# Kernel tuning notes

Measured on AMD Instinct MI355X. Metric: run time of the kernel, lower is better.

The kernel has to match this reference:

```python
import jax, jax.numpy as jnp
import numpy as np

D_MODEL = 1024
N_HEAD = 16
HEAD_SIZE = D_MODEL // N_HEAD
BLOCK_SIZE = 1024
NORM_EPS = 1e-6
B, T = 4, 1024


def setup_inputs() -> dict:
    key = jax.random.key(0)
    ks = jax.random.split(key, 16)
    s = 0.02
    d, h = D_MODEL, 4 * D_MODEL
    return {
        "x":  jax.random.normal(ks[0], (B, T, d), jnp.float32),
        "Wq": jax.random.normal(ks[1], (d, d), jnp.float32) * s,
        "bq": jax.random.normal(ks[2], (d,), jnp.float32) * s,
        "Wk": jax.random.normal(ks[3], (d, d), jnp.float32) * s,
        "bk": jax.random.normal(ks[4], (d,), jnp.float32) * s,
        "Wv": jax.random.normal(ks[5], (d, d), jnp.float32) * s,
        "bv": jax.random.normal(ks[6], (d,), jnp.float32) * s,
        "Wp": jax.random.normal(ks[7], (d, d), jnp.float32) * s,
        "bp": jax.random.normal(ks[8], (d,), jnp.float32) * s,
        "gamma": jnp.ones((d,), jnp.float32),
        "W1": jax.random.normal(ks[9], (d, h), jnp.float32) * s,
        "b1": jax.random.normal(ks[10], (h,), jnp.float32) * s,
        "W2": jax.random.normal(ks[11], (h, d), jnp.float32) * s,
        "b2": jax.random.normal(ks[12], (d,), jnp.float32) * s,
    }


def _rmsnorm(x, gamma):
    ms = jnp.mean(jnp.square(x), axis=-1, keepdims=True)
    return x * jax.lax.rsqrt(ms + NORM_EPS) * gamma


def _attn(x, Wq, bq, Wk, bk, Wv, bv, Wp, bp, causal):
    b, t, c = x.shape
    q = (x @ Wq + bq).reshape(b, t, N_HEAD, HEAD_SIZE)
    k = (x @ Wk + bk).reshape(b, t, N_HEAD, HEAD_SIZE)
    v = (x @ Wv + bv).reshape(b, t, N_HEAD, HEAD_SIZE)
    # NOTE: source divides by head_size**(-0.5) -> multiply by sqrt(head_size)
    scores = jnp.einsum("bqhd,bkhd->bhqk", q, k) * (HEAD_SIZE ** 0.5)
    if causal:
        tril = jnp.tril(jnp.ones((t, t), bool))
        scores = jnp.where(tril, scores, -jnp.inf)
    att = jax.nn.softmax(scores, axis=-1)
    out = jnp.einsum("bhqk,bkhd->bqhd", att, v).reshape(b, t, c)
    return out @ Wp + bp


def _ffwd(x, W1, b1, W2, b2):
    return jax.nn.leaky_relu(x @ W1 + b1, negative_slope=0.1) @ W2 + b2


def reference(x, Wq, bq, Wk, bk, Wv, bv, Wp, bp, gamma, W1, b1, W2, b2):
    # x_out = x + self_att(norm(x), mask=False)
    a = x + _attn(_rmsnorm(x, gamma), Wq, bq, Wk, bk, Wv, bv, Wp, bp, False)
    # x_out = x + ffwd(norm(x_out))   <- residual from ORIGINAL x (faithful)
    b = x + _ffwd(_rmsnorm(a, gamma), W1, b1, W2, b2)
    # x = x_out + self_att(norm(x_out), mask=True)
    c = b + _attn(_rmsnorm(b, gamma), Wq, bq, Wk, bk, Wv, bv, Wp, bp, True)
    return c
```

## Files before the change

### kernel.cpp

```cpp
#include <hip/hip_runtime.h>
#include <cstdint>
#include <cstddef>

typedef __bf16 bf16_t;
typedef __attribute__((ext_vector_type(8))) __bf16 bf16x8;
typedef __attribute__((ext_vector_type(4))) __bf16 bf16x4;
typedef __attribute__((ext_vector_type(4))) float f32x4;

constexpr int D  = 1024;
constexpr int TT = 1024;
constexpr int BB = 4;
constexpr int NH = 16;
constexpr int HS = 64;
constexpr int MR = BB * TT;
constexpr int HF = 4096;

__device__ inline void gload_lds16(const bf16_t* g, bf16_t* l)
{
    __builtin_amdgcn_global_load_lds(
        (const __attribute__((address_space(1))) void*)g,
        (__attribute__((address_space(3))) void*)l, 16, 0, 0);
}

template<bool LO>
__global__ __launch_bounds__(256) void rmsnorm_kernel(const float* __restrict__ x,
                                                      const float* __restrict__ gamma,
                                                      bf16_t* __restrict__ oh,
                                                      bf16_t* __restrict__ ol)
{
    int row = blockIdx.x;
    int t   = threadIdx.x;
    const float* xr = x + (size_t)row * D;
    float4 xv = *(const float4*)(xr + t * 4);
    float ss = xv.x * xv.x + xv.y * xv.y + xv.z * xv.z + xv.w * xv.w;
#pragma unroll
    for (int m = 1; m < 64; m <<= 1) ss += __shfl_xor(ss, m, 64);
    __shared__ float part[4];
    if ((t & 63) == 0) part[t >> 6] = ss;
    __syncthreads();
    float tot   = part[0] + part[1] + part[2] + part[3];
    float scale = rsqrtf(tot * (1.0f / D) + 1e-6f);
    float4 gv = *(const float4*)(gamma + t * 4);
    float vals[4] = {xv.x * scale * gv.x, xv.y * scale * gv.y,
                     xv.z * scale * gv.z, xv.w * scale * gv.w};
    bf16x4 vh, vl;
#pragma unroll
    for (int j = 0; j < 4; ++j) {
        bf16_t h = (bf16_t)vals[j];
        vh[j] = h;
        vl[j] = (bf16_t)(vals[j] - (float)h);
    }
    *(bf16x4*)(oh + (size_t)row * D + t * 4) = vh;
    if (LO) *(bf16x4*)(ol + (size_t)row * D + t * 4) = vl;
}

__global__ __launch_bounds__(256) void concat_bias_kernel(const float* __restrict__ a,
                                                          const float* __restrict__ b,
                                                          const float* __restrict__ c,
                                                          float* __restrict__ o)
{
    int i = blockIdx.x * 256 + threadIdx.x;
    o[i] = i < 1024 ? a[i] : (i < 2048 ? b[i - 1024] : c[i - 2048]);
}

template<bool LO>
__global__ __launch_bounds__(256) void convw_kernel(const float* __restrict__ W,
                                                    bf16_t* __restrict__ dH,
                                                    bf16_t* __restrict__ dL,
                                                    int K, int N)
{
    __shared__ float sld[64][65];
    int t = threadIdx.x;
    int k0 = blockIdx.x * 64, n0 = blockIdx.y * 64;
    int kr = t >> 4, nc = (t & 15) * 4;
#pragma unroll
    for (int p = 0; p < 4; ++p) {
        int k = p * 16 + kr;
        float4 v = *(const float4*)(W + (size_t)(k0 + k) * N + n0 + nc);
        sld[k][nc] = v.x; sld[k][nc + 1] = v.y; sld[k][nc + 2] = v.z; sld[k][nc + 3] = v.w;
    }
    __syncthreads();
    int n = t >> 2, kh = (t & 3) * 16;
    bf16x8 h0, l0, h1, l1;
#pragma unroll
    for (int j = 0; j < 8; ++j) {
        float v = sld[kh + j][n];
        bf16_t h = (bf16_t)v;
        h0[j] = h; l0[j] = (bf16_t)(v - (float)h);
    }
#pragma unroll
    for (int j = 0; j < 8; ++j) {
        float v = sld[kh + 8 + j][n];
        bf16_t h = (bf16_t)v;
        h1[j] = h; l1[j] = (bf16_t)(v - (float)h);
    }
    size_t o = (size_t)(n0 + n) * K + k0 + kh;
    *(bf16x8*)(dH + o)     = h0;
    *(bf16x8*)(dH + o + 8) = h1;
    if (LO) {
        *(bf16x8*)(dL + o)     = l0;
        *(bf16x8*)(dL + o + 8) = l1;
    }
}

template<int TN, bool CM, bool ALO, bool WLO, int OUTM, bool RELU, bool RESID>
__global__ __launch_bounds__(256, 2) void gemm_kernel(
    const bf16_t* __restrict__ Ahp, const bf16_t* __restrict__ Alp,
    const bf16_t* __restrict__ Whp, const bf16_t* __restrict__ Wlp,
    const float* __restrict__ bias, const float* resid,
    float* outf, bf16_t* __restrict__ outh, bf16_t* __restrict__ outl,
    int N, int K)
{
    constexpr int NF = TN / 32;
    constexpr int AP = ALO ? 2 : 1;
    constexpr int WP = WLO ? 2 : 1;
    __shared__ bf16_t sA[AP][128][32];
    __shared__ bf16_t sW[WP][TN][32];

    int t = threadIdx.x;
    int l = t & 63, w = t >> 6;
    int lr = l & 15, lg = l >> 4;

    int gx  = gridDim.x;
    int gy  = gridDim.y;
    int nwg = gx * gy;
    int bid = blockIdx.y * gx + blockIdx.x;
    int xcd = bid & 7, idx = bid >> 3;
    int nb, mb;
    if (CM) {
        int cw = gx >> 3;
        mb = idx % gy;
        nb = xcd * cw + idx / gy;
    } else {
        int s = xcd * (nwg >> 3) + idx;
        nb = s % gx; mb = s / gx;
    }
    int m0 = mb * 128, n0 = nb * TN;
    int wr = (w >> 1) * 64, wc = (w & 1) * (TN / 2);

    f32x4 acc[4][NF] = {};

    int srow = (l >> 2);
    int sch  = l & 3;

    for (int kk = 0; kk < K; kk += 32) {
        __syncthreads();
#pragma unroll
        for (int c = 0; c < 2; ++c) {
            int rbase = w * 32 + c * 16;
            int row = rbase + srow;
            int f = (row >> 1) & 3;
            size_t goff = (size_t)row * K + kk + (size_t)((sch ^ f)) * 8;
            gload_lds16(Ahp + (size_t)m0 * K + goff, &sA[0][rbase][0]);
            if (ALO) gload_lds16(Alp + (size_t)m0 * K + goff, &sA[AP - 1][rbase][0]);
        }
#pragma unroll
        for (int c = 0; c < TN / 64; ++c) {
            int rbase = w * (TN / 4) + c * 16;
            int row = rbase + srow;
            int f = (row >> 1) & 3;
            size_t goff = (size_t)row * K + kk + (size_t)((sch ^ f)) * 8;
            gload_lds16(Whp + (size_t)n0 * K + goff, &sW[0][rbase][0]);
            if (WLO) gload_lds16(Wlp + (size_t)n0 * K + goff, &sW[WP - 1][rbase][0]);
        }
        __syncthreads();

        bf16x8 a0[4], a1[4], b0[NF], b1[NF];
#pragma unroll
        for (int m = 0; m < 4; ++m) {
            int row = wr + m * 16 + lr;
            int sl = lg ^ ((row >> 1) & 3);
            a0[m] = *(const bf16x8*)&sA[0][row][sl * 8];
            if (ALO) a1[m] = *(const bf16x8*)&sA[AP - 1][row][sl * 8];
        }
#pragma unroll
        for (int n = 0; n < NF; ++n) {
            int row = wc + n * 16 + lr;
            int sl = lg ^ ((row >> 1) & 3);
            b0[n] = *(const bf16x8*)&sW[0][row][sl * 8];
            if (WLO) b1[n] = *(const bf16x8*)&sW[WP - 1][row][sl * 8];
        }
#pragma unroll
        for (int m = 0; m < 4; ++m)
#pragma unroll
            for (int n = 0; n < NF; ++n)
                acc[m][n] = __builtin_amdgcn_mfma_f32_16x16x32_bf16(a0[m], b0[n], acc[m][n], 0, 0, 0);
        if (WLO) {
#pragma unroll
            for (int m = 0; m < 4; ++m)
#pragma unroll
                for (int n = 0; n < NF; ++n)
                    acc[m][n] = __builtin_amdgcn_mfma_f32_16x16x32_bf16(a0[m], b1[n], acc[m][n], 0, 0, 0);
        }
        if (ALO) {
#pragma unroll
            for (int m = 0; m < 4; ++m)
#pragma unroll
                for (int n = 0; n < NF; ++n)
                    acc[m][n] = __builtin_amdgcn_mfma_f32_16x16x32_bf16(a1[m], b0[n], acc[m][n], 0, 0, 0);
        }
    }

#pragma unroll
    for (int m = 0; m < 4; ++m) {
#pragma unroll
        for (int n = 0; n < NF; ++n) {
            int col = n0 + wc + n * 16 + lr;
            float bv = bias[col];
#pragma unroll
            for (int r = 0; r < 4; ++r) {
                int row = m0 + wr + m * 16 + lg * 4 + r;
                float v = acc[m][n][r] + bv;
                if (RELU)  v = (v >= 0.0f) ? v : 0.1f * v;
                if (RESID) v += resid[(size_t)row * N + col];
                if (OUTM == 0) {
                    outf[(size_t)row * N + col] = v;
                } else if (OUTM == 2) {
                    outh[(size_t)row * N + col] = (bf16_t)v;
                } else {
                    bf16_t h = (bf16_t)v;
                    outh[(size_t)row * N + col] = h;
                    if (OUTM == 1 || col < 2048)
                        outl[(size_t)row * N + col] = (bf16_t)(v - (float)h);
                }
            }
        }
    }
}

template<bool CAUSAL>
__global__ __launch_bounds__(256, 2) void attn_kernel(
    const bf16_t* __restrict__ qkvH, const bf16_t* __restrict__ qkvL,
    bf16_t* __restrict__ oh)
{
    __shared__ bf16_t Vth[2][64][70];
    __shared__ bf16_t Ph[4][32][70];

    int tid = threadIdx.x;
    int b = blockIdx.z;
    int qb, h;
    if (CAUSAL) {
        int y = blockIdx.y;
        qb = (blockIdx.z & 2) ? (7 - (y & 7)) : (y & 7);
        h  = (blockIdx.x << 1) | (y >> 3);
    } else {
        h  = blockIdx.x;
        qb = blockIdx.y;
    }
    int l = tid & 63, w = tid >> 6;
    int lr = l & 15, lg = l >> 4;
    int qbase = qb * 128;
    const int QS = 3 * D;

    bf16x8 aqh[2][2], aql[2][2];
#pragma unroll
    for (int m = 0; m < 2; ++m) {
        size_t qoff = (size_t)(b * TT + qbase + w * 32 + m * 16 + lr) * QS + h * HS;
#pragma unroll
        for (int c = 0; c < 2; ++c) {
            aqh[m][c] = *(const bf16x8*)(qkvH + qoff + c * 32 + lg * 8);
            aql[m][c] = *(const bf16x8*)(qkvL + qoff + c * 32 + lg * 8);
        }
    }

    float mrow[2][4], lsum[2][4];
    f32x4 acc_o[2][4] = {};
#pragma unroll
    for (int m = 0; m < 2; ++m)
#pragma unroll
        for (int r = 0; r < 4; ++r) { mrow[m][r] = -1e30f; lsum[m][r] = 0.0f; }

    int ktmax = CAUSAL ? (2 * qb + 1) : (TT / 64 - 1);

    int vrow = tid >> 3;
    int vcol = (tid & 7) * 8;

    bf16x8 vreg[2];
#pragma unroll
    for (int rr = 0; rr < 2; ++rr)
        vreg[rr] = *(const bf16x8*)(qkvH + (size_t)(b * TT + vrow + rr * 32) * QS + 2 * D + h * HS + vcol);
#pragma unroll
    for (int rr = 0; rr < 2; ++rr)
#pragma unroll
        for (int j = 0; j < 8; ++j) Vth[0][vcol + j][vrow + rr * 32] = vreg[rr][j];

    bf16x8 kh0[4], kl0[4], kh1[4], kl1[4];
    {
        size_t koff = (size_t)(b * TT + lr) * QS + D + h * HS;
#pragma unroll
        for (int nt = 0; nt < 4; ++nt) {
            size_t ko = koff + (size_t)(nt * 16) * QS;
            kh0[nt] = *(const bf16x8*)(qkvH + ko + lg * 8);
            kl0[nt] = *(const bf16x8*)(qkvL + ko + lg * 8);
            kh1[nt] = *(const bf16x8*)(qkvH + ko + 32 + lg * 8);
            kl1[nt] = *(const bf16x8*)(qkvL + ko + 32 + lg * 8);
        }
    }
    __syncthreads();
    int cur = 0;

    for (int kt = 0; kt <= ktmax; ++kt) {
        int kbase = kt * 64;
        int ktn = kt < ktmax ? kt + 1 : ktmax;

#pragma unroll
        for (int rr = 0; rr < 2; ++rr)
            vreg[rr] = *(const bf16x8*)(qkvH + (size_t)(b * TT + ktn * 64 + vrow + rr * 32) * QS + 2 * D + h * HS + vcol);

        f32x4 accs[2][4];
#pragma unroll
        for (int nt = 0; nt < 4; ++nt) {
            __builtin_amdgcn_s_setprio(1);
#pragma unroll
            for (int m = 0; m < 2; ++m) {
                f32x4 s = {};
                s = __builtin_amdgcn_mfma_f32_16x16x32_bf16(aqh[m][0], kh0[nt], s, 0, 0, 0);
                s = __builtin_amdgcn_mfma_f32_16x16x32_bf16(aqh[m][0], kl0[nt], s, 0, 0, 0);
                s = __builtin_amdgcn_mfma_f32_16x16x32_bf16(aql[m][0], kh0[nt], s, 0, 0, 0);
                s = __builtin_amdgcn_mfma_f32_16x16x32_bf16(aqh[m][1], kh1[nt], s, 0, 0, 0);
                s = __builtin_amdgcn_mfma_f32_16x16x32_bf16(aqh[m][1], kl1[nt], s, 0, 0, 0);
                s = __builtin_amdgcn_mfma_f32_16x16x32_bf16(aql[m][1], kh1[nt], s, 0, 0, 0);
                accs[m][nt] = s * 8.0f;
            }
            __builtin_amdgcn_s_setprio(0);
        }

        {
            size_t koffn = (size_t)(b * TT + ktn * 64 + lr) * QS + D + h * HS;
#pragma unroll
            for (int nt = 0; nt < 4; ++nt) {
                size_t ko = koffn + (size_t)(nt * 16) * QS;
                kh0[nt] = *(const bf16x8*)(qkvH + ko + lg * 8);
                kl0[nt] = *(const bf16x8*)(qkvL + ko + lg * 8);
                kh1[nt] = *(const bf16x8*)(qkvH + ko + 32 + lg * 8);
                kl1[nt] = *(const bf16x8*)(qkvL + ko + 32 + lg * 8);
            }
        }

        if (CAUSAL && kt >= 2 * qb) {
#pragma unroll
            for (int m = 0; m < 2; ++m)
#pragma unroll
                for (int nt = 0; nt < 4; ++nt)
#pragma unroll
                    for (int r = 0; r < 4; ++r) {
                        int qrow = qbase + w * 32 + m * 16 + lg * 4 + r;
                        int kcol = kbase + nt * 16 + lr;
                        if (kcol > qrow) accs[m][nt][r] = -1e30f;
                    }
        }

#pragma unroll
        for (int m = 0; m < 2; ++m) {
            float alpha[4];
#pragma unroll
            for (int r = 0; r < 4; ++r) {
                float mx = fmaxf(fmaxf(accs[m][0][r], accs[m][1][r]),
                                 fmaxf(accs[m][2][r], accs[m][3][r]));
#pragma unroll
                for (int msk = 1; msk < 16; msk <<= 1) mx = fmaxf(mx, __shfl_xor(mx, msk, 64));
                float mnew = fmaxf(mrow[m][r], mx);
                float sum = 0.0f;
#pragma unroll
                for (int nt = 0; nt < 4; ++nt) {
                    float p = __expf(accs[m][nt][r] - mnew);
                    accs[m][nt][r] = p;
                    sum += p;
                }
#pragma unroll
                for (int msk = 1; msk < 16; msk <<= 1) sum += __shfl_xor(sum, msk, 64);
                alpha[r] = __expf(mrow[m][r] - mnew);
                lsum[m][r] = lsum[m][r] * alpha[r] + sum;
                mrow[m][r] = mnew;
            }
#pragma unroll
            for (int et = 0; et < 4; ++et)
#pragma unroll
                for (int r = 0; r < 4; ++r) acc_o[m][et][r] *= alpha[r];

#pragma unroll
            for (int nt = 0; nt < 4; ++nt)
#pragma unroll
                for (int r = 0; r < 4; ++r)
                    Ph[w][m * 16 + lg * 4 + r][nt * 16 + lr] = (bf16_t)accs[m][nt][r];
        }

#pragma unroll
        for (int m = 0; m < 2; ++m) {
            bf16x8 ap0 = *(const bf16x8*)&Ph[w][m * 16 + lr][lg * 8];
            bf16x8 ap1 = *(const bf16x8*)&Ph[w][m * 16 + lr][32 + lg * 8];
            __builtin_amdgcn_s_setprio(1);
#pragma unroll
            for (int et = 0; et < 4; ++et) {
                bf16x8 bv0 = *(const bf16x8*)&Vth[cur][et * 16 + lr][lg * 8];
                bf16x8 bv1 = *(const bf16x8*)&Vth[cur][et * 16 + lr][32 + lg * 8];
                acc_o[m][et] = __builtin_amdgcn_mfma_f32_16x16x32_bf16(ap0, bv0, acc_o[m][et], 0, 0, 0);
                acc_o[m][et] = __builtin_amdgcn_mfma_f32_16x16x32_bf16(ap1, bv1, acc_o[m][et], 0, 0, 0);
            }
            __builtin_amdgcn_s_setprio(0);
        }

#pragma unroll
        for (int rr = 0; rr < 2; ++rr)
#pragma unroll
            for (int j = 0; j < 8; ++j) Vth[cur ^ 1][vcol + j][vrow + rr * 32] = vreg[rr][j];
        __syncthreads();
        cur ^= 1;
    }

#pragma unroll
    for (int m = 0; m < 2; ++m) {
        size_t obase = (size_t)(b * TT + qbase + w * 32 + m * 16) * D + h * HS;
#pragma unroll
        for (int r = 0; r < 4; ++r) {
            float inv = 1.0f / lsum[m][r];
#pragma unroll
            for (int et = 0; et < 4; ++et) {
                float v = acc_o[m][et][r] * inv;
                size_t idx = obase + (size_t)(lg * 4 + r) * D + et * 16 + lr;
                oh[idx] = (bf16_t)v;
            }
        }
    }
}

extern "C" void kernel_launch(void* const* d_in, const int* in_sizes, int n_in,
                              void* d_out, int out_size, void* d_ws, size_t ws_size,
                              hipStream_t stream)
{
    const float* x     = (const float*)d_in[0];
    const float* Wq    = (const float*)d_in[1];
    const float* bq    = (const float*)d_in[2];
    const float* Wk    = (const float*)d_in[3];
    const float* bk    = (const float*)d_in[4];
    const float* Wv    = (const float*)d_in[5];
    const float* bv    = (const float*)d_in[6];
    const float* Wp    = (const float*)d_in[7];
    const float* bp    = (const float*)d_in[8];
    const float* gamma = (const float*)d_in[9];
    const float* W1    = (const float*)d_in[10];
    const float* b1    = (const float*)d_in[11];
    const float* W2    = (const float*)d_in[12];
    const float* b2    = (const float*)d_in[13];
    float* out = (float*)d_out;

    char* base = (char*)d_ws;
    bf16_t* nrmH  = (bf16_t*)(base);
    bf16_t* nrmL  = (bf16_t*)(base + (8u  << 20));
    bf16_t* qkvH  = (bf16_t*)(base + (16u << 20));
    bf16_t* qkvL  = (bf16_t*)(base + (40u << 20));
    bf16_t* h1H   = (bf16_t*)(base + (16u << 20));
    bf16_t* w1sl  = (bf16_t*)(base + (48u << 20));
    float*  bias3 = (float*)(base + (64u << 20));
    bf16_t* w2sl  = (bf16_t*)(base + (64u << 20));
    bf16_t* wsl   = (bf16_t*)(base + (80u << 20));
    bf16_t* aoH = nrmH;
    float* abuf = out;
    float* bbuf = out;

    size_t DD = (size_t)D * D;
    bf16_t* wqkvH = wsl;
    bf16_t* wqkvL = wsl + 3 * DD;
    bf16_t* wpH   = wsl + 6 * DD;
    bf16_t* wpL   = wsl + 7 * DD;

    dim3 blk(256);
    dim3 gcvD(D / 64, D / 64);
    dim3 gcv1(D / 64, HF / 64);
    dim3 gcv2(HF / 64, D / 64);
    dim3 gQKV(3 * D / 128, MR / 128);
    dim3 gP(D / 64, MR / 128);
    dim3 gF(HF / 128, MR / 128);
    dim3 gAnc(NH, TT / 128, BB);
    dim3 gAc(TT / 128, NH, BB);

    rmsnorm_kernel<true><<<MR, blk, 0, stream>>>(x, gamma, nrmH, nrmL);
    concat_bias_kernel<<<12, blk, 0, stream>>>(bq, bk, bv, bias3);
    convw_kernel<true><<<gcvD, blk, 0, stream>>>(Wq, wqkvH,          wqkvL,          D, D);
    convw_kernel<true><<<gcvD, blk, 0, stream>>>(Wk, wqkvH + DD,     wqkvL + DD,     D, D);
    convw_kernel<true><<<gcvD, blk, 0, stream>>>(Wv, wqkvH + 2 * DD, wqkvL + 2 * DD, D, D);
    convw_kernel<true><<<gcvD, blk, 0, stream>>>(Wp, wpH,            wpL,            D, D);
    gemm_kernel<128, false, true, true, 3, false, false><<<gQKV, blk, 0, stream>>>(nrmH, nrmL, wqkvH, wqkvL, bias3, nullptr, nullptr, qkvH, qkvL, 3 * D, D);
    attn_kernel<false><<<gAnc, blk, 0, stream>>>(qkvH, qkvL, aoH);
    gemm_kernel<64, false, false, true, 0, false, true><<<gP, blk, 0, stream>>>(aoH, nullptr, wpH, wpL, bp, x, abuf, nullptr, nullptr, D, D);

    rmsnorm_kernel<false><<<MR, blk, 0, stream>>>(abuf, gamma, nrmH, nullptr);
    convw_kernel<false><<<gcv1, blk, 0, stream>>>(W1, w1sl, nullptr, D, HF);
    gemm_kernel<128, true, false, false, 2, true, false><<<gF, blk, 0, stream>>>(nrmH, nullptr, w1sl, nullptr, b1, nullptr, nullptr, h1H, nullptr, HF, D);
    convw_kernel<false><<<gcv2, blk, 0, stream>>>(W2, w2sl, nullptr, HF, D);
    gemm_kernel<64, false, false, false, 0, false, true><<<gP, blk, 0, stream>>>(h1H, nullptr, w2sl, nullptr, b2, x, bbuf, nullptr, nullptr, D, HF);

    rmsnorm_kernel<true><<<MR, blk, 0, stream>>>(bbuf, gamma, nrmH, nrmL);
    concat_bias_kernel<<<12, blk, 0, stream>>>(bq, bk, bv, bias3);
    gemm_kernel<128, false, true, true, 3, false, false><<<gQKV, blk, 0, stream>>>(nrmH, nrmL, wqkvH, wqkvL, bias3, nullptr, nullptr, qkvH, qkvL, 3 * D, D);
    attn_kernel<true><<<gAc, blk, 0, stream>>>(qkvH, qkvL, aoH);
    gemm_kernel<64, false, false, true, 0, false, true><<<gP, blk, 0, stream>>>(aoH, nullptr, wpH, wpL, bp, bbuf, out, nullptr, nullptr, D, D);
}
```

Measured before the change: 522.7 us.

## Split V projection out of QKV GEMM and drop low-bf16 terms for V and Wp

The fused QKV projection becomes a split-precision QK GEMM plus a separate single-bf16 V GEMM writing its own buffer, and the attention kernel reads V from that buffer. The Wv and Wp weights are now converted only to high bf16 parts, and the output projection GEMM drops the low-weight correction term. This removes the extra MFMA passes and low-part memory traffic for V and the projections, at the cost of lower accuracy on those paths and one extra kernel launch per attention block.

```diff
diff --git a/kernel.cpp b/kernel.cpp
--- a/kernel.cpp
+++ b/kernel.cpp
@@ -56,11 +56,10 @@
 
 __global__ __launch_bounds__(256) void concat_bias_kernel(const float* __restrict__ a,
                                                           const float* __restrict__ b,
-                                                          const float* __restrict__ c,
                                                           float* __restrict__ o)
 {
     int i = blockIdx.x * 256 + threadIdx.x;
-    o[i] = i < 1024 ? a[i] : (i < 2048 ? b[i - 1024] : c[i - 2048]);
+    o[i] = i < 1024 ? a[i] : b[i - 1024];
 }
 
 template<bool LO>
@@ -220,8 +219,7 @@
                 } else {
                     bf16_t h = (bf16_t)v;
                     outh[(size_t)row * N + col] = h;
-                    if (OUTM == 1 || col < 2048)
-                        outl[(size_t)row * N + col] = (bf16_t)(v - (float)h);
+                    outl[(size_t)row * N + col] = (bf16_t)(v - (float)h);
                 }
             }
         }
@@ -230,8 +228,8 @@
 
 template<bool CAUSAL>
 __global__ __launch_bounds__(256, 2) void attn_kernel(
-    const bf16_t* __restrict__ qkvH, const bf16_t* __restrict__ qkvL,
-    bf16_t* __restrict__ oh)
+    const bf16_t* __restrict__ qkH, const bf16_t* __restrict__ qkL,
+    const bf16_t* __restrict__ vP, bf16_t* __restrict__ oh)
 {
     __shared__ bf16_t Vth[2][64][70];
     __shared__ bf16_t Ph[4][32][70];
@@ -250,16 +248,16 @@
     int l = tid & 63, w = tid >> 6;
     int lr = l & 15, lg = l >> 4;
     int qbase = qb * 128;
-    const int QS = 3 * D;
+    const int QKS = 2 * D;
 
     bf16x8 aqh[2][2], aql[2][2];
 #pragma unroll
     for (int m = 0; m < 2; ++m) {
-        size_t qoff = (size_t)(b * TT + qbase + w * 32 + m * 16 + lr) * QS + h * HS;
+        size_t qoff = (size_t)(b * TT + qbase + w * 32 + m * 16 + lr) * QKS + h * HS;
 #pragma unroll
         for (int c = 0; c < 2; ++c) {
-            aqh[m][c] = *(const bf16x8*)(qkvH + qoff + c * 32 + lg * 8);
-            aql[m][c] = *(const bf16x8*)(qkvL + qoff + c * 32 + lg * 8);
+            aqh[m][c] = *(const bf16x8*)(qkH + qoff + c * 32 + lg * 8);
+            aql[m][c] = *(const bf16x8*)(qkL + qoff + c * 32 + lg * 8);
         }
     }
 
@@ -278,7 +276,7 @@
     bf16x8 vreg[2];
 #pragma unroll
     for (int rr = 0; rr < 2; ++rr)
-        vreg[rr] = *(const bf16x8*)(qkvH + (size_t)(b * TT + vrow + rr * 32) * QS + 2 * D + h * HS + vcol);
+        vreg[rr] = *(const bf16x8*)(vP + (size_t)(b * TT + vrow + rr * 32) * D + h * HS + vcol);
 #pragma unroll
     for (int rr = 0; rr < 2; ++rr)
 #pragma unroll
@@ -286,14 +284,14 @@
 
     bf16x8 kh0[4], kl0[4], kh1[4], kl1[4];
     {
-        size_t koff = (size_t)(b * TT + lr) * QS + D + h * HS;
+        size_t koff = (size_t)(b * TT + lr) * QKS + D + h * HS;
 #pragma unroll
         for (int nt = 0; nt < 4; ++nt) {
-            size_t ko = koff + (size_t)(nt * 16) * QS;
-            kh0[nt] = *(const bf16x8*)(qkvH + ko + lg * 8);
-            kl0[nt] = *(const bf16x8*)(qkvL + ko + lg * 8);
-            kh1[nt] = *(const bf16x8*)(qkvH + ko + 32 + lg * 8);
-            kl1[nt] = *(const bf16x8*)(qkvL + ko + 32 + lg * 8);
+            size_t ko = koff + (size_t)(nt * 16) * QKS;
+            kh0[nt] = *(const bf16x8*)(qkH + ko + lg * 8);
+            kl0[nt] = *(const bf16x8*)(qkL + ko + lg * 8);
+            kh1[nt] = *(const bf16x8*)(qkH + ko + 32 + lg * 8);
+            kl1[nt] = *(const bf16x8*)(qkL + ko + 32 + lg * 8);
         }
     }
     __syncthreads();
@@ -305,7 +303,7 @@
 
 #pragma unroll
         for (int rr = 0; rr < 2; ++rr)
-            vreg[rr] = *(const bf16x8*)(qkvH + (size_t)(b * TT + ktn * 64 + vrow + rr * 32) * QS + 2 * D + h * HS + vcol);
+            vreg[rr] = *(const bf16x8*)(vP + (size_t)(b * TT + ktn * 64 + vrow + rr * 32) * D + h * HS + vcol);
 
         f32x4 accs[2][4];
 #pragma unroll
@@ -326,14 +324,14 @@
         }
 
         {
-            size_t koffn = (size_t)(b * TT + ktn * 64 + lr) * QS + D + h * HS;
+            size_t koffn = (size_t)(b * TT + ktn * 64 + lr) * QKS + D + h * HS;
 #pragma unroll
             for (int nt = 0; nt < 4; ++nt) {
-                size_t ko = koffn + (size_t)(nt * 16) * QS;
-                kh0[nt] = *(const bf16x8*)(qkvH + ko + lg * 8);
-                kl0[nt] = *(const bf16x8*)(qkvL + ko + lg * 8);
-                kh1[nt] = *(const bf16x8*)(qkvH + ko + 32 + lg * 8);
-                kl1[nt] = *(const bf16x8*)(qkvL + ko + 32 + lg * 8);
+                size_t ko = koffn + (size_t)(nt * 16) * QKS;
+                kh0[nt] = *(const bf16x8*)(qkH + ko + lg * 8);
+                kl0[nt] = *(const bf16x8*)(qkL + ko + lg * 8);
+                kh1[nt] = *(const bf16x8*)(qkH + ko + 32 + lg * 8);
+                kl1[nt] = *(const bf16x8*)(qkL + ko + 32 + lg * 8);
             }
         }
 
@@ -447,11 +445,12 @@
     char* base = (char*)d_ws;
     bf16_t* nrmH  = (bf16_t*)(base);
     bf16_t* nrmL  = (bf16_t*)(base + (8u  << 20));
-    bf16_t* qkvH  = (bf16_t*)(base + (16u << 20));
-    bf16_t* qkvL  = (bf16_t*)(base + (40u << 20));
+    bf16_t* qkH   = (bf16_t*)(base + (16u << 20));
+    bf16_t* qkL   = (bf16_t*)(base + (32u << 20));
+    bf16_t* vH    = (bf16_t*)(base + (48u << 20));
     bf16_t* h1H   = (bf16_t*)(base + (16u << 20));
     bf16_t* w1sl  = (bf16_t*)(base + (48u << 20));
-    float*  bias3 = (float*)(base + (64u << 20));
+    float*  bias2 = (float*)(base + (64u << 20));
     bf16_t* w2sl  = (bf16_t*)(base + (64u << 20));
     bf16_t* wsl   = (bf16_t*)(base + (80u << 20));
     bf16_t* aoH = nrmH;
@@ -459,30 +458,31 @@
     float* bbuf = out;
 
     size_t DD = (size_t)D * D;
-    bf16_t* wqkvH = wsl;
-    bf16_t* wqkvL = wsl + 3 * DD;
-    bf16_t* wpH   = wsl + 6 * DD;
-    bf16_t* wpL   = wsl + 7 * DD;
+    bf16_t* wqkH = wsl;
+    bf16_t* wqkL = wsl + 2 * DD;
+    bf16_t* wvH  = wsl + 4 * DD;
+    bf16_t* wpH  = wsl + 5 * DD;
 
     dim3 blk(256);
     dim3 gcvD(D / 64, D / 64);
     dim3 gcv1(D / 64, HF / 64);
     dim3 gcv2(HF / 64, D / 64);
-    dim3 gQKV(3 * D / 128, MR / 128);
+    dim3 gQK(2 * D / 128, MR / 128);
     dim3 gP(D / 64, MR / 128);
     dim3 gF(HF / 128, MR / 128);
     dim3 gAnc(NH, TT / 128, BB);
     dim3 gAc(TT / 128, NH, BB);
 
     rmsnorm_kernel<true><<<MR, blk, 0, stream>>>(x, gamma, nrmH, nrmL);
-    concat_bias_kernel<<<12, blk, 0, stream>>>(bq, bk, bv, bias3);
-    convw_kernel<true><<<gcvD, blk, 0, stream>>>(Wq, wqkvH,          wqkvL,          D, D);
-    convw_kernel<true><<<gcvD, blk, 0, stream>>>(Wk, wqkvH + DD,     wqkvL + DD,     D, D);
-    convw_kernel<true><<<gcvD, blk, 0, stream>>>(Wv, wqkvH + 2 * DD, wqkvL + 2 * DD, D, D);
-    convw_kernel<true><<<gcvD, blk, 0, stream>>>(Wp, wpH,            wpL,            D, D);
-    gemm_kernel<128, false, true, true, 3, false, false><<<gQKV, blk, 0, stream>>>(nrmH, nrmL, wqkvH, wqkvL, bias3, nullptr, nullptr, qkvH, qkvL, 3 * D, D);
-    attn_kernel<false><<<gAnc, blk, 0, stream>>>(qkvH, qkvL, aoH);
-    gemm_kernel<64, false, false, true, 0, false, true><<<gP, blk, 0, stream>>>(aoH, nullptr, wpH, wpL, bp, x, abuf, nullptr, nullptr, D, D);
+    concat_bias_kernel<<<8, blk, 0, stream>>>(bq, bk, bias2);
+    convw_kernel<true><<<gcvD, blk, 0, stream>>>(Wq, wqkH,      wqkL,      D, D);
+    convw_kernel<true><<<gcvD, blk, 0, stream>>>(Wk, wqkH + DD, wqkL + DD, D, D);
+    convw_kernel<false><<<gcvD, blk, 0, stream>>>(Wv, wvH, nullptr, D, D);
+    convw_kernel<false><<<gcvD, blk, 0, stream>>>(Wp, wpH, nullptr, D, D);
+    gemm_kernel<128, false, true, true, 1, false, false><<<gQK, blk, 0, stream>>>(nrmH, nrmL, wqkH, wqkL, bias2, nullptr, nullptr, qkH, qkL, 2 * D, D);
+    gemm_kernel<64, false, false, false, 2, false, false><<<gP, blk, 0, stream>>>(nrmH, nullptr, wvH, nullptr, bv, nullptr, nullptr, vH, nullptr, D, D);
+    attn_kernel<false><<<gAnc, blk, 0, stream>>>(qkH, qkL, vH, aoH);
+    gemm_kernel<64, false, false, false, 0, false, true><<<gP, blk, 0, stream>>>(aoH, nullptr, wpH, nullptr, bp, x, abuf, nullptr, nullptr, D, D);
 
     rmsnorm_kernel<false><<<MR, blk, 0, stream>>>(abuf, gamma, nrmH, nullptr);
     convw_kernel<false><<<gcv1, blk, 0, stream>>>(W1, w1sl, nullptr, D, HF);
@@ -491,8 +491,9 @@
     gemm_kernel<64, false, false, false, 0, false, true><<<gP, blk, 0, stream>>>(h1H, nullptr, w2sl, nullptr, b2, x, bbuf, nullptr, nullptr, D, HF);
 
     rmsnorm_kernel<true><<<MR, blk, 0, stream>>>(bbuf, gamma, nrmH, nrmL);
-    concat_bias_kernel<<<12, blk, 0, stream>>>(bq, bk, bv, bias3);
-    gemm_kernel<128, false, true, true, 3, false, false><<<gQKV, blk, 0, stream>>>(nrmH, nrmL, wqkvH, wqkvL, bias3, nullptr, nullptr, qkvH, qkvL, 3 * D, D);
-    attn_kernel<true><<<gAc, blk, 0, stream>>>(qkvH, qkvL, aoH);
-    gemm_kernel<64, false, false, true, 0, false, true><<<gP, blk, 0, stream>>>(aoH, nullptr, wpH, wpL, bp, bbuf, out, nullptr, nullptr, D, D);
-}
+    concat_bias_kernel<<<8, blk, 0, stream>>>(bq, bk, bias2);
+    gemm_kernel<128, false, true, true, 1, false, false><<<gQK, blk, 0, stream>>>(nrmH, nrmL, wqkH, wqkL, bias2, nullptr, nullptr, qkH, qkL, 2 * D, D);
+    gemm_kernel<64, false, false, false, 2, false, false><<<gP, blk, 0, stream>>>(nrmH, nullptr, wvH, nullptr, bv, nullptr, nullptr, vH, nullptr, D, D);
+    attn_kernel<true><<<gAc, blk, 0, stream>>>(qkH, qkL, vH, aoH);
+    gemm_kernel<64, false, false, false, 0, false, true><<<gP, blk, 0, stream>>>(aoH, nullptr, wpH, nullptr, bp, bbuf, out, nullptr, nullptr, D, D);
+}
```

After: 500.5 us, median of 2. -4.2%, faster.
